# Optimization experiments

Hardware: AMD Instinct MI355X
Metric: run time of the kernel (lower is better)

Reference implementation:

```python
import jax, jax.numpy as jnp
import numpy as np
from jax import lax

EPS = 1e-5

# Straight-through identity binarization (torch code mutates .data, so autograd
# sees binarized values but grads flow as identity to the latent weights/inputs).
def ste_sign(x):
    return x + lax.stop_gradient(jnp.sign(x) - x)

# SignActivation: sign forward, hard-tanh-style gradient (zero where |i| > 1).
@jax.custom_vjp
def sign_act(x):
    return jnp.sign(x)

def _sa_fwd(x):
    return jnp.sign(x), x

def _sa_bwd(x, g):
    return (jnp.where(jnp.abs(x) <= 1.0, g, 0.0),)

sign_act.defvjp(_sa_fwd, _sa_bwd)

def bn2d(x, gamma, beta):
    # training-mode BatchNorm2d: batch stats over (N,H,W), biased variance
    mean = jnp.mean(x, axis=(0, 2, 3), keepdims=True)
    var = jnp.var(x, axis=(0, 2, 3), keepdims=True)
    xn = (x - mean) * lax.rsqrt(var + EPS)
    return xn * gamma.reshape(1, -1, 1, 1) + beta.reshape(1, -1, 1, 1)

def bn1d(x, gamma, beta):
    mean = jnp.mean(x, axis=0, keepdims=True)
    var = jnp.var(x, axis=0, keepdims=True)
    xn = (x - mean) * lax.rsqrt(var + EPS)
    return xn * gamma[None, :] + beta[None, :]

def conv2d(x, w, stride, pad):
    return lax.conv_general_dilated(
        x, w, window_strides=(stride, stride),
        padding=((pad, pad), (pad, pad)),
        dimension_numbers=("NCHW", "OIHW", "NCHW"))


def setup_inputs() -> dict:
    key = jax.random.key(0)
    ks = jax.random.split(key, 4)
    width = 0.01
    x = jax.random.normal(ks[0], (8192, 1, 28, 28), dtype=jnp.float32)
    w1 = jax.random.normal(ks[1], (32, 1, 5, 5), dtype=jnp.float32) * width
    w2 = jax.random.normal(ks[2], (64, 32, 4, 4), dtype=jnp.float32) * width
    w3 = jax.random.normal(ks[3], (10, 64 * 64), dtype=jnp.float32) * width
    g1 = jnp.ones((32,), jnp.float32); b1 = jnp.zeros((32,), jnp.float32)
    g2 = jnp.ones((64,), jnp.float32); b2 = jnp.zeros((64,), jnp.float32)
    g3 = jnp.ones((10,), jnp.float32); b3 = jnp.zeros((10,), jnp.float32)
    return {"x": x, "w1": w1, "g1": g1, "b1": b1,
            "w2": w2, "g2": g2, "b2": b2,
            "w3": w3, "g3": g3, "b3": b3}


def reference(x, w1, g1, b1, w2, g2, b2, w3, g3, b3):
    # cv1: input channels = 1 != 3 -> input binarized; weight binarized
    h = conv2d(ste_sign(x), ste_sign(w1), stride=2, pad=2)   # [B,32,14,14]
    h = bn2d(h, g1, b1)
    h = sign_act(h)
    # cv2: input channels 32 != 3 -> binarized (no-op on +-1 values)
    h = conv2d(ste_sign(h), ste_sign(w2), stride=2, pad=2)   # [B,64,8,8]
    h = bn2d(h, g2, b2)
    h = sign_act(h)
    h = h.reshape(h.shape[0], -1)                            # [B,4096]
    # fc3: features 4096 != 784 -> binarized (no-op on +-1 values)
    h = jnp.dot(ste_sign(h), ste_sign(w3).T)                 # [B,10]
    h = bn1d(h, g3, b3)
    return h
```

## Files before the change

### kernel.cpp

```cpp
#include <hip/hip_runtime.h>
#include <stdint.h>


#define NB 8192
typedef unsigned long long ull;

#define OFF_C1  ((size_t)0)
#define SZ_C1   ((size_t)NB*6272)
#define OFF_C2  (OFF_C1 + SZ_C1)
#define SZ_C2   ((size_t)NB*4096)
#define OFF_FC  (OFF_C2 + SZ_C2)
#define SZ_FC   ((size_t)NB*10*4)
#define OFF_S1  (OFF_FC + SZ_FC)
#define OFF_S2  (OFF_S1 + 2048)
#define OFF_S3  (OFF_S2 + 8192)
#define OFF_W2B (OFF_S3 + 2048)
#define OFF_W3B (OFF_W2B + 4096)

__device__ inline void mk_thresh(double s, double t, int &T, int &flip) {
    if (s > 0.0) {
        int v = (int)floor(-t / s) - 2;
        for (int c = 0; c < 6; ++c) { if (s * (double)v + t > 0.0) break; ++v; }
        T = v; flip = 0;
    } else if (s < 0.0) {
        int v = (int)floor(-t / s) - 2;
        for (int c = 0; c < 6; ++c) { if (!(s * (double)v + t > 0.0)) break; ++v; }
        T = v; flip = 1;
    } else { T = -200; flip = (t > 0.0) ? 0 : 1; }
}
__device__ inline int clampT(int T, int lim) {
    return (T < -lim) ? -lim : (T > lim) ? lim : T;
}

__global__ __launch_bounds__(256) void kA_conv1(
    const float* __restrict__ x, const float* __restrict__ w1,
    const float* __restrict__ w2, const float* __restrict__ w3,
    int8_t* __restrict__ c1out, int* __restrict__ stats1,
    ull* __restrict__ w2bT, ull* __restrict__ w3b)
{
    const int tid = threadIdx.x, lane = tid & 63, wv = tid >> 6;

    if (blockIdx.x >= 2048) {
        const int t = (blockIdx.x - 2048)*256 + tid;
        if (t < 512) {
            const int idx = t >> 6, k = t & 63;
            const int u = idx >> 1, pr = idx & 1;
            uint32_t lo = 0u, hi = 0u;
            #pragma unroll 8
            for (int c = 0; c < 32; ++c) {
                const float* wp = w2 + (((k*32 + c)*4 + u)*4 + 2*pr);
                lo |= (wp[0] > 0.f ? 1u : 0u) << c;
                hi |= (wp[1] > 0.f ? 1u : 0u) << c;
            }
            w2bT[t] = (ull)lo | ((ull)hi << 32);
        } else if (t < 1152) {
            const int w = t - 512;
            const float* wp = w3 + (size_t)(w >> 6)*4096 + (size_t)(w & 63)*64;
            ull bits = 0ull;
            #pragma unroll 16
            for (int k = 0; k < 64; ++k)
                bits |= (ull)(wp[k] > 0.f ? 1 : 0) << k;
            w3b[w] = bits;
        }
        return;
    }

    __shared__ ull sxb[4][16];
    __shared__ uint32_t wfilt[32];
    __shared__ uint32_t outb[4][1568];
    __shared__ int lsum[32], lsq[32];

    if (tid < 32) {
        uint32_t f = 0u;
        #pragma unroll
        for (int q = 0; q < 25; ++q) f |= (w1[tid*25 + q] > 0.f ? 1u : 0u) << q;
        wfilt[tid] = f;
        lsum[tid] = 0; lsq[tid] = 0;
    }
    __syncthreads();
    const int n = blockIdx.x*4 + wv;
    #pragma unroll
    for (int t = 0; t < 13; ++t) {
        const int idx = t*64 + lane;
        const float v = (idx < 784) ? x[(size_t)n*784 + idx] : -1.f;
        const ull bal = __ballot(v > 0.f);
        if (lane == t) sxb[wv][t] = bal;
    }
    if (lane == 13) sxb[wv][13] = 0ull;
    for (int t = 0; t < 4; ++t) {
        const int p = t*64 + lane;
        if (p < 196) {
            const int i = p / 14, j = p - i*14;
            const uint32_t cmask = (j == 0) ? 0x1Cu : (j == 13) ? 0x0Fu : 0x1Fu;
            uint32_t win = 0u, vm = 0u;
            #pragma unroll
            for (int u = 0; u < 5; ++u) {
                const int r = 2*i + u - 2;
                if (r >= 0 && r < 28) {
                    const int bp = 28*r, w0 = bp >> 6, sh = bp & 63;
                    const ull a = sxb[wv][w0], b = sxb[wv][w0+1];
                    uint32_t row = (uint32_t)((a >> sh) | ((b << 1) << (63 - sh)));
                    row = (row & 0x0FFFFFFFu) << 2;
                    win |= ((row >> (2*j)) & 31u) << (5*u);
                    vm  |= cmask << (5*u);
                }
            }
            const int nv = __popc(vm);
            uint32_t dw[8];
            #pragma unroll
            for (int d = 0; d < 8; ++d) dw[d] = 0u;
            #pragma unroll
            for (int c = 0; c < 32; ++c) {
                const int diff = __popc((win ^ wfilt[c]) & vm);
                const int o = nv - 2*diff;
                dw[c >> 2] |= (uint32_t)(o & 255) << (8*(c & 3));
            }
            #pragma unroll
            for (int d = 0; d < 8; ++d) outb[wv][p*8 + d] = dw[d];
        }
    }
    {
        int4* dst = (int4*)(c1out + (size_t)n*6272);
        const int4* src = (const int4*)&outb[wv][0];
        #pragma unroll
        for (int t = 0; t < 7; ++t) {
            const int idx = t*64 + lane;
            if (idx < 392) dst[idx] = src[idx];
        }
    }
    {
        int s4[4] = {0,0,0,0}, q4[4] = {0,0,0,0};
        const uint32_t* ob32 = &outb[wv][0];
        #pragma unroll
        for (int t = 0; t < 25; ++t) {
            const int idx = t*64 + lane;
            if (idx < 1568) {
                const uint32_t dwv = ob32[idx];
                #pragma unroll
                for (int qq = 0; qq < 4; ++qq) {
                    const int v = (int)((int8_t)(dwv >> (8*qq)));
                    s4[qq] += v; q4[qq] += v*v;
                }
            }
        }
        #pragma unroll
        for (int off = 8; off <= 32; off <<= 1) {
            #pragma unroll
            for (int qq = 0; qq < 4; ++qq) {
                s4[qq] += __shfl_xor(s4[qq], off);
                q4[qq] += __shfl_xor(q4[qq], off);
            }
        }
        if (lane < 8) {
            #pragma unroll
            for (int qq = 0; qq < 4; ++qq) {
                atomicAdd(&lsum[lane*4 + qq], s4[qq]);
                atomicAdd(&lsq[lane*4 + qq], q4[qq]);
            }
        }
    }
    __syncthreads();
    if (tid < 32) {
        const int shard = blockIdx.x & 7;
        atomicAdd(&stats1[(shard*32 + tid)*2 + 0], lsum[tid]);
        atomicAdd(&stats1[(shard*32 + tid)*2 + 1], lsq[tid]);
    }
}

__global__ __launch_bounds__(256) void kB_conv2(
    const int8_t* __restrict__ c1out, const int* __restrict__ stats1,
    const float* __restrict__ gm1, const float* __restrict__ bt1,
    const ull* __restrict__ w2bT,
    ull* __restrict__ c2out, ull* __restrict__ stats2)
{
    __shared__ uint32_t BwU[4][14][16];
    __shared__ int sT1[32];
    __shared__ uint32_t sFlip1;
    __shared__ int ssum[64], ssq[64];
    const int tid = threadIdx.x, lane = tid & 63, wv = tid >> 6;
    const int n = blockIdx.x*4 + wv;

    uint32_t Wlo[8], Whi[8];
    #pragma unroll
    for (int idx = 0; idx < 8; ++idx) {
        const uint2 w = ((const uint2*)w2bT)[idx*64 + lane];
        Wlo[idx] = w.x; Whi[idx] = w.y;
    }

    if (tid < 64) { ssum[tid] = 0; ssq[tid] = 0; }
    int fl = 0;
    if (tid < 32) {
        long long s = 0, q = 0;
        for (int sh = 0; sh < 8; ++sh) {
            s += stats1[(sh*32 + tid)*2 + 0];
            q += stats1[(sh*32 + tid)*2 + 1];
        }
        const double N = 8192.0 * 196.0;
        const double mean = (double)s / N;
        const double var  = (double)q / N - mean*mean;
        const double a = (double)gm1[tid] / sqrt(var + 1e-5);
        const double b = (double)bt1[tid] - mean*a;
        int T; mk_thresh(a, b, T, fl);
        sT1[tid] = clampT(T, 26);
    }
    if (wv == 0) {
        const uint32_t fn1 = ~(uint32_t)__ballot(fl != 0);
        if (lane == 0) sFlip1 = fn1;
    }
    __syncthreads();
    const uint32_t flipn1 = sFlip1;

    for (int t = lane; t < 196; t += 64) {
        const int r = t / 14, c = t - r*14;
        const uint4* src = (const uint4*)(c1out + ((size_t)n*196 + t)*32);
        const uint4 lo4 = src[0], hi4 = src[1];
        const uint32_t wsrc[8] = {lo4.x, lo4.y, lo4.z, lo4.w, hi4.x, hi4.y, hi4.z, hi4.w};
        uint32_t neg = 0u;
        #pragma unroll
        for (int d = 0; d < 8; ++d) {
            #pragma unroll
            for (int qq = 0; qq < 4; ++qq) {
                const int ch = d*4 + qq;
                const int v = (int)((int8_t)(wsrc[d] >> (8*qq)));
                neg |= ((uint32_t)(v - sT1[ch]) >> 31) << ch;
            }
        }
        BwU[wv][r][c] = neg ^ flipn1;
    }

    uint32_t PA[32], PB[32];
#define LOADP(BUF, K)                                                          \
    {                                                                          \
        const uint4* r0 = (const uint4*)&BwU[wv][2*(K)][0];                    \
        const uint4* r1 = (const uint4*)&BwU[wv][2*(K)+1][0];                  \
        _Pragma("unroll")                                                      \
        for (int tt = 0; tt < 4; ++tt) {                                       \
            const uint4 v0 = r0[tt];                                           \
            BUF[4*tt+0] = v0.x; BUF[4*tt+1] = v0.y;                            \
            BUF[4*tt+2] = v0.z; BUF[4*tt+3] = v0.w;                            \
            const uint4 v1 = r1[tt];                                           \
            BUF[16+4*tt+0] = v1.x; BUF[16+4*tt+1] = v1.y;                      \
            BUF[16+4*tt+2] = v1.z; BUF[16+4*tt+3] = v1.w;                      \
        }                                                                      \
    }
#define UT(BUF, RO, UU)                                                        \
    {                                                                          \
        if (j >= 1) { D += __popc(BUF[(RO)*16 + 2*j-2] ^ Wlo[2*(UU)])          \
                         + __popc(BUF[(RO)*16 + 2*j-1] ^ Whi[2*(UU)]);   ++nw; } \
        if (j <= 6) { D += __popc(BUF[(RO)*16 + 2*j]   ^ Wlo[2*(UU)+1])        \
                         + __popc(BUF[(RO)*16 + 2*j+1] ^ Whi[2*(UU)+1]); ++nw; } \
    }
    int s = 0, q = 0;
    ull* dst = c2out + (size_t)n*512 + lane;
    LOADP(PA, 0)
    #pragma unroll
    for (int i = 0; i < 8; ++i) {
        if (i >= 1 && i <= 6) {
            if (i & 1) { LOADP(PB, i) } else { LOADP(PA, i) }
        }
        uint32_t o0 = 0u, o1 = 0u;
        #pragma unroll
        for (int j = 0; j < 8; ++j) {
            int D = 0, nw = 0;
            if (i >= 1) {
                if ((i-1) & 1) { UT(PB, 0, 0) UT(PB, 1, 1) }
                else           { UT(PA, 0, 0) UT(PA, 1, 1) }
            }
            if (i <= 6) {
                if (i & 1) { UT(PB, 0, 2) UT(PB, 1, 3) }
                else       { UT(PA, 0, 2) UT(PA, 1, 3) }
            }
            const int o = 32*nw - D;
            s += o; q += o*o;
            if (j < 4) o0 |= (uint32_t)(o & 255) << (8*j);
            else       o1 |= (uint32_t)(o & 255) << (8*(j-4));
        }
        dst[i*64] = (ull)o0 | ((ull)o1 << 32);
    }
#undef LOADP
#undef UT
    atomicAdd(&ssum[lane], s);
    atomicAdd(&ssq[lane], q);
    __syncthreads();
    if (tid < 64) {
        const int shard = blockIdx.x & 7;
        atomicAdd(&stats2[(shard*64 + tid)*2 + 0], (ull)(long long)ssum[tid]);
        atomicAdd(&stats2[(shard*64 + tid)*2 + 1], (ull)(long long)ssq[tid]);
    }
}

__global__ __launch_bounds__(256) void kC_fc(
    const ull* __restrict__ c2o, const float* __restrict__ gm2,
    const float* __restrict__ bt2, const ull* __restrict__ stats2,
    const ull* __restrict__ w3b,
    int* __restrict__ fc, ull* __restrict__ stats3)
{
    __shared__ int fco[4][10];
    __shared__ int s3[10], q3[10];
    __shared__ int sT2[64];
    __shared__ ull sFlip2;
    const int tid = threadIdx.x, lane = tid & 63, wv = tid >> 6;
    if (tid < 10) { s3[tid] = 0; q3[tid] = 0; }
    if (wv == 0) {
        long long ss = 0, qq = 0;
        for (int sh = 0; sh < 8; ++sh) {
            ss += (long long)stats2[(sh*64 + lane)*2 + 0];
            qq += (long long)stats2[(sh*64 + lane)*2 + 1];
        }
        const double N = 8192.0 * 64.0;
        const double mh = (double)ss / N;
        const double vh = (double)qq / N - mh*mh;
        const double a = (double)gm2[lane] / sqrt(4.0*vh + 1e-5);
        const double b = (double)bt2[lane] - 2.0*mh*a;
        int T, fl; mk_thresh(2.0*a, b, T, fl);
        sT2[lane] = clampT(T, 200);
        const ull fn2 = ~__ballot(fl != 0);
        if (lane == 0) sFlip2 = fn2;
    }
    __syncthreads();
    const int T2 = sT2[lane];
    const ull flipn2 = sFlip2;
    const int n = blockIdx.x*4 + wv;
    const ull* src = c2o + (size_t)n*512 + lane;
    uint32_t neglo = 0u, neghi = 0u;
    #pragma unroll
    for (int ii = 0; ii < 8; ++ii) {
        const ull v8 = src[(size_t)ii*64];
        const uint32_t w0 = (uint32_t)v8, w1 = (uint32_t)(v8 >> 32);
        uint32_t b8 = 0u;
        #pragma unroll
        for (int b = 0; b < 4; ++b) {
            const int v0 = (int)((int8_t)(w0 >> (8*b)));
            b8 |= ((uint32_t)(v0 - T2) >> 31) << b;
            const int v1 = (int)((int8_t)(w1 >> (8*b)));
            b8 |= ((uint32_t)(v1 - T2) >> 31) << (4 + b);
        }
        if (ii < 4) neglo |= b8 << (8*ii); else neghi |= b8 << (8*(ii-4));
    }
    const ull myw = ((ull)neglo | ((ull)neghi << 32)) ^ flipn2;
    uint32_t pk[5];
    #pragma unroll
    for (int t = 0; t < 5; ++t) {
        const uint32_t pa = (uint32_t)__popcll(myw ^ w3b[(2*t+0)*64 + lane]);
        const uint32_t pb = (uint32_t)__popcll(myw ^ w3b[(2*t+1)*64 + lane]);
        pk[t] = pa | (pb << 16);
    }
    #pragma unroll
    for (int off = 32; off >= 1; off >>= 1) {
        #pragma unroll
        for (int t = 0; t < 5; ++t) pk[t] += __shfl_xor(pk[t], off);
    }
    if (lane == 0) {
        #pragma unroll
        for (int m = 0; m < 10; ++m) {
            const int tot = (pk[m >> 1] >> (16*(m & 1))) & 0xFFFF;
            fco[wv][m] = 4096 - 2*tot;
        }
    }
    __syncthreads();
    if (tid < 40) {
        const int li = tid / 10, m = tid - li*10;
        const int o = fco[li][m];
        fc[(size_t)(blockIdx.x*4 + li)*10 + m] = o;
        atomicAdd(&s3[m], o);
        atomicAdd(&q3[m], o*o);
    }
    __syncthreads();
    if (tid < 10) {
        const int shard = blockIdx.x & 7;
        atomicAdd(&stats3[(shard*10 + tid)*2 + 0], (ull)(long long)s3[tid]);
        atomicAdd(&stats3[(shard*10 + tid)*2 + 1], (ull)(long long)q3[tid]);
    }
}

__global__ __launch_bounds__(256) void kD_apply(
    const int* __restrict__ fc, const float* __restrict__ gm3,
    const float* __restrict__ bt3, const ull* __restrict__ stats3,
    float* __restrict__ out)
{
    __shared__ float a3[10], b3[10];
    const int tid = threadIdx.x;
    if (tid < 10) {
        long long s = 0, q = 0;
        for (int sh = 0; sh < 8; ++sh) {
            s += (long long)stats3[(sh*10 + tid)*2 + 0];
            q += (long long)stats3[(sh*10 + tid)*2 + 1];
        }
        const double N = 8192.0;
        const double mean = (double)s / N;
        const double var  = (double)q / N - mean*mean;
        const double a = (double)gm3[tid] / sqrt(var + 1e-5);
        a3[tid] = (float)a;
        b3[tid] = (float)((double)bt3[tid] - mean*a);
    }
    __syncthreads();
    const int e = blockIdx.x*256 + tid;
    if (e < NB*10) {
        const int m = e % 10;
        out[e] = fmaf(a3[m], (float)fc[e], b3[m]);
    }
}

extern "C" void kernel_launch(void* const* d_in, const int* in_sizes, int n_in,
                              void* d_out, int out_size, void* d_ws, size_t ws_size,
                              hipStream_t stream)
{
    const float* x   = (const float*)d_in[0];
    const float* w1  = (const float*)d_in[1];
    const float* gm1 = (const float*)d_in[2];
    const float* bt1 = (const float*)d_in[3];
    const float* w2  = (const float*)d_in[4];
    const float* gm2 = (const float*)d_in[5];
    const float* bt2 = (const float*)d_in[6];
    const float* w3  = (const float*)d_in[7];
    const float* gm3 = (const float*)d_in[8];
    const float* bt3 = (const float*)d_in[9];
    char* ws = (char*)d_ws;
    int8_t* c1o = (int8_t*)(ws + OFF_C1);
    ull*    c2o = (ull*)(ws + OFF_C2);
    int*    fcb = (int*)(ws + OFF_FC);
    int*    s1  = (int*)(ws + OFF_S1);
    ull*    s2  = (ull*)(ws + OFF_S2);
    ull*    s3  = (ull*)(ws + OFF_S3);
    ull*    w2bp = (ull*)(ws + OFF_W2B);
    ull*    w3bp = (ull*)(ws + OFF_W3B);

    (void)hipMemsetAsync(ws + OFF_S1, 0, 12288, stream);
    kA_conv1<<<2053, 256, 0, stream>>>(x, w1, w2, w3, c1o, s1, w2bp, w3bp);
    kB_conv2<<<2048, 256, 0, stream>>>(c1o, s1, gm1, bt1, w2bp, c2o, s2);
    kC_fc   <<<2048, 256, 0, stream>>>(c2o, gm2, bt2, s2, w3bp, fcb, s3);
    kD_apply<<<320,  256, 0, stream>>>(fcb, gm3, bt3, s3, (float*)d_out);
}
```

Baseline: 182.6 us.

## Recompute conv1 in conv2 kernel instead of storing int8 intermediate

Conv1 no longer writes its int8 outputs (about 51 MB) to global memory; it only accumulates batch-norm statistics. The conv2 kernel re-reads the input x, rebinarizes it with ballots, and recomputes the conv1 popcount results before thresholding. This trades a large global write plus read for redundant conv1 arithmetic and a second read of x.

```diff
diff --git a/kernel.cpp b/kernel.cpp
--- a/kernel.cpp
+++ b/kernel.cpp
@@ -5,9 +5,7 @@
 #define NB 8192
 typedef unsigned long long ull;
 
-#define OFF_C1  ((size_t)0)
-#define SZ_C1   ((size_t)NB*6272)
-#define OFF_C2  (OFF_C1 + SZ_C1)
+#define OFF_C2  ((size_t)0)
 #define SZ_C2   ((size_t)NB*4096)
 #define OFF_FC  (OFF_C2 + SZ_C2)
 #define SZ_FC   ((size_t)NB*10*4)
@@ -35,7 +33,7 @@
 __global__ __launch_bounds__(256) void kA_conv1(
     const float* __restrict__ x, const float* __restrict__ w1,
     const float* __restrict__ w2, const float* __restrict__ w3,
-    int8_t* __restrict__ c1out, int* __restrict__ stats1,
+    int* __restrict__ stats1,
     ull* __restrict__ w2bT, ull* __restrict__ w3b)
 {
     const int tid = threadIdx.x, lane = tid & 63, wv = tid >> 6;
@@ -120,15 +118,6 @@
         }
     }
     {
-        int4* dst = (int4*)(c1out + (size_t)n*6272);
-        const int4* src = (const int4*)&outb[wv][0];
-        #pragma unroll
-        for (int t = 0; t < 7; ++t) {
-            const int idx = t*64 + lane;
-            if (idx < 392) dst[idx] = src[idx];
-        }
-    }
-    {
         int s4[4] = {0,0,0,0}, q4[4] = {0,0,0,0};
         const uint32_t* ob32 = &outb[wv][0];
         #pragma unroll
@@ -168,11 +157,14 @@
 }
 
 __global__ __launch_bounds__(256) void kB_conv2(
-    const int8_t* __restrict__ c1out, const int* __restrict__ stats1,
+    const float* __restrict__ x, const float* __restrict__ w1,
+    const int* __restrict__ stats1,
     const float* __restrict__ gm1, const float* __restrict__ bt1,
     const ull* __restrict__ w2bT,
     ull* __restrict__ c2out, ull* __restrict__ stats2)
 {
+    __shared__ ull sxb[4][16];
+    __shared__ uint32_t wfilt[32];
     __shared__ uint32_t BwU[4][14][16];
     __shared__ int sT1[32];
     __shared__ uint32_t sFlip1;
@@ -190,6 +182,10 @@
     if (tid < 64) { ssum[tid] = 0; ssq[tid] = 0; }
     int fl = 0;
     if (tid < 32) {
+        uint32_t f = 0u;
+        #pragma unroll
+        for (int q = 0; q < 25; ++q) f |= (w1[tid*25 + q] > 0.f ? 1u : 0u) << q;
+        wfilt[tid] = f;
         long long s = 0, q = 0;
         for (int sh = 0; sh < 8; ++sh) {
             s += stats1[(sh*32 + tid)*2 + 0];
@@ -207,25 +203,42 @@
         const uint32_t fn1 = ~(uint32_t)__ballot(fl != 0);
         if (lane == 0) sFlip1 = fn1;
     }
+    #pragma unroll
+    for (int t = 0; t < 13; ++t) {
+        const int idx = t*64 + lane;
+        const float v = (idx < 784) ? x[(size_t)n*784 + idx] : -1.f;
+        const ull bal = __ballot(v > 0.f);
+        if (lane == t) sxb[wv][t] = bal;
+    }
+    if (lane == 13) sxb[wv][13] = 0ull;
     __syncthreads();
     const uint32_t flipn1 = sFlip1;
 
     for (int t = lane; t < 196; t += 64) {
-        const int r = t / 14, c = t - r*14;
-        const uint4* src = (const uint4*)(c1out + ((size_t)n*196 + t)*32);
-        const uint4 lo4 = src[0], hi4 = src[1];
-        const uint32_t wsrc[8] = {lo4.x, lo4.y, lo4.z, lo4.w, hi4.x, hi4.y, hi4.z, hi4.w};
+        const int i = t / 14, j = t - i*14;
+        const uint32_t cmask = (j == 0) ? 0x1Cu : (j == 13) ? 0x0Fu : 0x1Fu;
+        uint32_t win = 0u, vm = 0u;
+        #pragma unroll
+        for (int u = 0; u < 5; ++u) {
+            const int r = 2*i + u - 2;
+            if (r >= 0 && r < 28) {
+                const int bp = 28*r, w0 = bp >> 6, sh = bp & 63;
+                const ull a = sxb[wv][w0], b = sxb[wv][w0+1];
+                uint32_t row = (uint32_t)((a >> sh) | ((b << 1) << (63 - sh)));
+                row = (row & 0x0FFFFFFFu) << 2;
+                win |= ((row >> (2*j)) & 31u) << (5*u);
+                vm  |= cmask << (5*u);
+            }
+        }
+        const int nv = __popc(vm);
         uint32_t neg = 0u;
         #pragma unroll
-        for (int d = 0; d < 8; ++d) {
-            #pragma unroll
-            for (int qq = 0; qq < 4; ++qq) {
-                const int ch = d*4 + qq;
-                const int v = (int)((int8_t)(wsrc[d] >> (8*qq)));
-                neg |= ((uint32_t)(v - sT1[ch]) >> 31) << ch;
-            }
-        }
-        BwU[wv][r][c] = neg ^ flipn1;
+        for (int c = 0; c < 32; ++c) {
+            const int diff = __popc((win ^ wfilt[c]) & vm);
+            const int o = nv - 2*diff;
+            neg |= ((uint32_t)(o - sT1[c]) >> 31) << c;
+        }
+        BwU[wv][i][j] = neg ^ flipn1;
     }
 
     uint32_t PA[32], PB[32];
@@ -416,7 +429,6 @@
     const float* gm3 = (const float*)d_in[8];
     const float* bt3 = (const float*)d_in[9];
     char* ws = (char*)d_ws;
-    int8_t* c1o = (int8_t*)(ws + OFF_C1);
     ull*    c2o = (ull*)(ws + OFF_C2);
     int*    fcb = (int*)(ws + OFF_FC);
     int*    s1  = (int*)(ws + OFF_S1);
@@ -426,8 +438,8 @@
     ull*    w3bp = (ull*)(ws + OFF_W3B);
 
     (void)hipMemsetAsync(ws + OFF_S1, 0, 12288, stream);
-    kA_conv1<<<2053, 256, 0, stream>>>(x, w1, w2, w3, c1o, s1, w2bp, w3bp);
-    kB_conv2<<<2048, 256, 0, stream>>>(c1o, s1, gm1, bt1, w2bp, c2o, s2);
+    kA_conv1<<<2053, 256, 0, stream>>>(x, w1, w2, w3, s1, w2bp, w3bp);
+    kB_conv2<<<2048, 256, 0, stream>>>(x, w1, s1, gm1, bt1, w2bp, c2o, s2);
     kC_fc   <<<2048, 256, 0, stream>>>(c2o, gm2, bt2, s2, w3bp, fcb, s3);
     kD_apply<<<320,  256, 0, stream>>>(fcb, gm3, bt3, s3, (float*)d_out);
 }
```

Measured after the change: 190.9 us. +4.5%, slower.
